# Performance work log

Hardware: AMD Instinct MI355X
Metric: run time of the kernel (lower is better)

Reference implementation:

```python
import jax, jax.numpy as jnp
import numpy as np

B, T, F, H = 2048, 512, 60, 7  # batch, seq_len, input_size, hidden_size


def setup_inputs() -> dict:
    key = jax.random.key(0)
    ks = jax.random.split(key, 9)
    bound = 1.0 / np.sqrt(H)  # PyTorch LSTM init: U(-1/sqrt(H), 1/sqrt(H))
    u = lambda k, s: jax.random.uniform(k, s, jnp.float32, -bound, bound)
    return {
        "x": jax.random.normal(ks[0], (B, T, F), jnp.float32),
        "Wih0": u(ks[1], (4 * H, F)),
        "Whh0": u(ks[2], (4 * H, H)),
        "bih0": u(ks[3], (4 * H,)),
        "bhh0": u(ks[4], (4 * H,)),
        "Wih1": u(ks[5], (4 * H, H)),
        "Whh1": u(ks[6], (4 * H, H)),
        "bih1": u(ks[7], (4 * H,)),
        "bhh1": u(ks[8], (4 * H,)),
    }


def _cell(xt, h, c, Wih, Whh, b):
    # PyTorch gate order: input, forget, cell(g), output
    gates = xt @ Wih.T + h @ Whh.T + b  # [B, 4H]
    i, f, g, o = jnp.split(gates, 4, axis=-1)
    c_new = jax.nn.sigmoid(f) * c + jax.nn.sigmoid(i) * jnp.tanh(g)
    h_new = jax.nn.sigmoid(o) * jnp.tanh(c_new)
    return h_new, c_new


def reference(x, Wih0, Whh0, bih0, bhh0, Wih1, Whh1, bih1, bhh1):
    b0 = bih0 + bhh0
    b1 = bih1 + bhh1
    batch = x.shape[0]
    hid = Whh0.shape[1]
    z = jnp.zeros((batch, hid), x.dtype)

    def step(carry, xt):
        h0, c0, h1, c1 = carry
        h0, c0 = _cell(xt, h0, c0, Wih0, Whh0, b0)
        h1, c1 = _cell(h0, h1, c1, Wih1, Whh1, b1)
        return (h0, c0, h1, c1), None

    xs = jnp.swapaxes(x, 0, 1)  # [T, B, F] for scan over time
    (h0, c0, h1, c1), _ = jax.lax.scan(step, (z, z, z, z), xs)
    # out[:, -1] of batch_first LSTM == final hidden state of top layer
    return h1
```

## Files before the change

kernel.cpp:

```cpp
#include <hip/hip_runtime.h>


#define B_ 2048
#define T_ 512
#define F_ 60
#define H_ 7
#define G4 28
#define CH 16
#define NCH (T_ / CH)
#define F4 15
#define ROW4 (CH * F4)
#define BPB 4
#define TOT4 (BPB * ROW4)
#define L2E 1.4426950408889634f

#if __has_builtin(__builtin_amdgcn_exp2f)
#define EXP2(x) __builtin_amdgcn_exp2f(x)
#else
#define EXP2(x) exp2f(x)
#endif

__device__ __forceinline__ float rcpf_(float v) { return __builtin_amdgcn_rcpf(v); }

__device__ __forceinline__ float bcast(float v, int srclane) {
    return __uint_as_float(__builtin_amdgcn_readlane(__float_as_uint(v), srclane));
}

__device__ __forceinline__ float dot7(const float* w, const float* h, float seed) {
    float m01 = fmaf(w[1], h[1], w[0] * h[0]);
    float m23 = fmaf(w[3], h[3], w[2] * h[2]);
    float m45 = fmaf(w[5], h[5], w[4] * h[4]);
    float m6  = fmaf(w[6], h[6], seed);
    return (m01 + m23) + (m45 + m6);
}

__device__ __forceinline__ float proj32(const float* pw, const float4* rp, float seed) {
    float s0 = seed, s1 = 0.f, s2 = 0.f, s3 = 0.f;
    #pragma unroll
    for (int j = 0; j < 8; ++j) {
        float4 q = rp[j];
        s0 = fmaf(pw[4 * j + 0], q.x, s0);
        s1 = fmaf(pw[4 * j + 1], q.y, s1);
        s2 = fmaf(pw[4 * j + 2], q.z, s2);
        s3 = fmaf(pw[4 * j + 3], q.w, s3);
    }
    return (s0 + s1) + (s2 + s3);
}

__global__ __launch_bounds__(256, 2)
void lstm2_kernel(const float* __restrict__ x,
                  const float* __restrict__ Wih0, const float* __restrict__ Whh0,
                  const float* __restrict__ bih0, const float* __restrict__ bhh0,
                  const float* __restrict__ Wih1, const float* __restrict__ Whh1,
                  const float* __restrict__ bih1, const float* __restrict__ bhh1,
                  float* __restrict__ out)
{
    __shared__ float4 lds4[2][BPB][ROW4];

    const int tid   = threadIdx.x;
    const int lane  = tid & 63;
    const bool isL1 = lane >= 32;
    const int g     = lane & 31;
    const int u     = g;
    const int r     = (g < G4) ? g : (G4 - 1);
    const int grp   = tid >> 6;
    const int b     = blockIdx.x * BPB + grp;

    float pw[32];
    {
        const int offs = isL1 ? 28 : 0;
        #pragma unroll
        for (int k = 0; k < 32; ++k) pw[k] = Wih0[r * F_ + offs + k];
        if (isL1) { pw[0] = pw[1] = pw[2] = pw[3] = 0.f; }
    }
    float wA[H_], wB[H_];
    #pragma unroll
    for (int v = 0; v < H_; ++v) {
        wA[v] = isL1 ? Wih1[r * H_ + v] : Whh0[r * H_ + v];
        wB[v] = isL1 ? Whh1[r * H_ + v] : 0.f;
    }
    const float bias0 = bih0[r] + bhh0[r];
    const float bias1 = bih1[r] + bhh1[r];

    const bool isT = (r >= 2 * H_ && r < 3 * H_);
    const float KK = isT ? (-2.f * L2E) : (-L2E);
    const float Aa = isT ? 2.f : 1.f;
    const float Ca = isT ? -1.f : 0.f;

    float h0v[H_] = {0, 0, 0, 0, 0, 0, 0};
    float h1v[H_] = {0, 0, 0, 0, 0, 0, 0};
    float c = 0.f;
    float hnew = 0.f;

    const float4* __restrict__ xb =
        (const float4*)(x + (size_t)(blockIdx.x * BPB) * T_ * F_);
    const int XB4 = T_ * F4;
    const int lofs = isL1 ? 7 : 0;
    const float pseed = isL1 ? 0.f : bias0;

    #pragma unroll
    for (int i = 0; i < 4; ++i) {
        int idx = tid + 256 * i;
        if (idx < TOT4) {
            int bl = idx / ROW4;
            int j  = idx - bl * ROW4;
            lds4[0][bl][j] = xb[bl * XB4 + j];
        }
    }
    __syncthreads();

    float a_in;
    {
        float ow = proj32(pw, &lds4[0][grp][0] + lofs, pseed);
        a_in = ow + __shfl(ow, lane ^ 32, 64);
    }

    for (int ch = 0; ch < NCH; ++ch) {
        const int cn = (ch < NCH - 1) ? ch + 1 : ch;
        float4 st[4];
        #pragma unroll
        for (int i = 0; i < 4; ++i) {
            int idx = tid + 256 * i;
            if (idx < TOT4) {
                int bl = idx / ROW4;
                int j  = idx - bl * ROW4;
                st[i] = xb[bl * XB4 + cn * ROW4 + j];
            }
        }

        const int buf = ch & 1;
        const float4* __restrict__ rowb = &lds4[buf][grp][0] + lofs;

        #pragma unroll
        for (int s = 0; s < CH; ++s) {
            float seed = isL1 ? bias1 : a_in;
            float a = dot7(wA, h0v, seed);
            a = dot7(wB, h1v, a);
            float act = fmaf(Aa, rcpf_(1.f + EXP2(KK * a)), Ca);

            float fg = __shfl(act, lane + 7, 64);
            float gg = __shfl(act, lane + 14, 64);
            float og = __shfl(act, lane + 21, 64);

            float cnew = fmaf(fg, c, act * gg);
            if (ch == 0 && s == 0) cnew = isL1 ? 0.f : cnew;
            c = cnew;
            float th = fmaf(2.f, rcpf_(1.f + EXP2(-2.f * L2E * c)), -1.f);
            hnew = og * th;

            #pragma unroll
            for (int v = 0; v < H_; ++v) h0v[v] = bcast(hnew, v);
            if (ch > 0 || s > 0) {
                #pragma unroll
                for (int v = 0; v < H_; ++v) h1v[v] = bcast(hnew, 32 + v);
            }

            if (s < CH - 1) {
                float ow = proj32(pw, rowb + (s + 1) * F4, pseed);
                a_in = ow + __shfl(ow, lane ^ 32, 64);
            }
        }

        #pragma unroll
        for (int i = 0; i < 4; ++i) {
            int idx = tid + 256 * i;
            if (idx < TOT4) {
                int bl = idx / ROW4;
                int j  = idx - bl * ROW4;
                lds4[buf ^ 1][bl][j] = st[i];
            }
        }
        __syncthreads();

        if (ch < NCH - 1) {
            float ow = proj32(pw, &lds4[buf ^ 1][grp][0] + lofs, pseed);
            a_in = ow + __shfl(ow, lane ^ 32, 64);
        }
    }

    {
        float seed = isL1 ? bias1 : 0.f;
        float a = dot7(wA, h0v, seed);
        a = dot7(wB, h1v, a);
        float act = fmaf(Aa, rcpf_(1.f + EXP2(KK * a)), Ca);
        float fg = __shfl(act, lane + 7, 64);
        float gg = __shfl(act, lane + 14, 64);
        float og = __shfl(act, lane + 21, 64);
        c = fmaf(fg, c, act * gg);
        float th = fmaf(2.f, rcpf_(1.f + EXP2(-2.f * L2E * c)), -1.f);
        hnew = og * th;
    }

    if (isL1 && u < H_) {
        out[(size_t)b * H_ + u] = hnew;
    }
}

extern "C" void kernel_launch(void* const* d_in, const int* in_sizes, int n_in,
                              void* d_out, int out_size, void* d_ws, size_t ws_size,
                              hipStream_t stream) {
    const float* x    = (const float*)d_in[0];
    const float* Wih0 = (const float*)d_in[1];
    const float* Whh0 = (const float*)d_in[2];
    const float* bih0 = (const float*)d_in[3];
    const float* bhh0 = (const float*)d_in[4];
    const float* Wih1 = (const float*)d_in[5];
    const float* Whh1 = (const float*)d_in[6];
    const float* bih1 = (const float*)d_in[7];
    const float* bhh1 = (const float*)d_in[8];
    float* out = (float*)d_out;

    dim3 grid(B_ / BPB);
    dim3 block(256);
    lstm2_kernel<<<grid, block, 0, stream>>>(x, Wih0, Whh0, bih0, bhh0,
                                             Wih1, Whh1, bih1, bhh1, out);
}
```

Before: 569.8 us.

## Split input projection into a parallel pre-pass kernel before the recurrence

```diff
diff --git a/kernel.cpp b/kernel.cpp
--- a/kernel.cpp
+++ b/kernel.cpp
@@ -6,13 +6,9 @@
 #define F_ 60
 #define H_ 7
 #define G4 28
-#define CH 16
-#define NCH (T_ / CH)
-#define F4 15
-#define ROW4 (CH * F4)
-#define BPB 4
-#define TOT4 (BPB * ROW4)
+#define BT_ (B_ * T_)
 #define L2E 1.4426950408889634f
+#define PD 8
 
 #if __has_builtin(__builtin_amdgcn_exp2f)
 #define EXP2(x) __builtin_amdgcn_exp2f(x)
@@ -34,52 +30,71 @@
     return (m01 + m23) + (m45 + m6);
 }
 
-__device__ __forceinline__ float proj32(const float* pw, const float4* rp, float seed) {
-    float s0 = seed, s1 = 0.f, s2 = 0.f, s3 = 0.f;
-    #pragma unroll
-    for (int j = 0; j < 8; ++j) {
-        float4 q = rp[j];
-        s0 = fmaf(pw[4 * j + 0], q.x, s0);
-        s1 = fmaf(pw[4 * j + 1], q.y, s1);
-        s2 = fmaf(pw[4 * j + 2], q.z, s2);
-        s3 = fmaf(pw[4 * j + 3], q.w, s3);
-    }
-    return (s0 + s1) + (s2 + s3);
-}
-
-__global__ __launch_bounds__(256, 2)
-void lstm2_kernel(const float* __restrict__ x,
-                  const float* __restrict__ Wih0, const float* __restrict__ Whh0,
-                  const float* __restrict__ bih0, const float* __restrict__ bhh0,
-                  const float* __restrict__ Wih1, const float* __restrict__ Whh1,
-                  const float* __restrict__ bih1, const float* __restrict__ bhh1,
-                  float* __restrict__ out)
+__global__ __launch_bounds__(256)
+void proj_kernel(const float* __restrict__ x, const float* __restrict__ Wih0,
+                 const float* __restrict__ bih0, const float* __restrict__ bhh0,
+                 float* __restrict__ A)
 {
-    __shared__ float4 lds4[2][BPB][ROW4];
-
+    __shared__ float wsm[G4 * F_];
+    __shared__ float bsm[G4];
+
+    for (int i = threadIdx.x; i < G4 * F_; i += 256) wsm[i] = Wih0[i];
+    if (threadIdx.x < G4) bsm[threadIdx.x] = bih0[threadIdx.x] + bhh0[threadIdx.x];
+    __syncthreads();
+
+    const int bt = blockIdx.x * 256 + threadIdx.x;
+
+    float xr[F_];
+    const float4* __restrict__ xp = (const float4*)(x + (size_t)bt * F_);
+    #pragma unroll
+    for (int j = 0; j < 15; ++j) {
+        float4 q = xp[j];
+        xr[4 * j + 0] = q.x; xr[4 * j + 1] = q.y;
+        xr[4 * j + 2] = q.z; xr[4 * j + 3] = q.w;
+    }
+
+    float4* __restrict__ Ap = (float4*)(A + (size_t)bt * G4);
+    #pragma unroll
+    for (int rg = 0; rg < 7; ++rg) {
+        float s[4];
+        #pragma unroll
+        for (int q = 0; q < 4; ++q) {
+            const int r = rg * 4 + q;
+            const float* w = &wsm[r * F_];
+            float a0 = bsm[r], a1 = 0.f, a2 = 0.f, a3 = 0.f;
+            #pragma unroll
+            for (int k = 0; k < F_; k += 4) {
+                a0 = fmaf(w[k + 0], xr[k + 0], a0);
+                a1 = fmaf(w[k + 1], xr[k + 1], a1);
+                a2 = fmaf(w[k + 2], xr[k + 2], a2);
+                a3 = fmaf(w[k + 3], xr[k + 3], a3);
+            }
+            s[q] = (a0 + a1) + (a2 + a3);
+        }
+        Ap[rg] = make_float4(s[0], s[1], s[2], s[3]);
+    }
+}
+
+__global__ __launch_bounds__(256)
+void rec_kernel(const float* __restrict__ A,
+                const float* __restrict__ Whh0,
+                const float* __restrict__ Wih1, const float* __restrict__ Whh1,
+                const float* __restrict__ bih1, const float* __restrict__ bhh1,
+                float* __restrict__ out)
+{
     const int tid   = threadIdx.x;
     const int lane  = tid & 63;
     const bool isL1 = lane >= 32;
     const int g     = lane & 31;
-    const int u     = g;
     const int r     = (g < G4) ? g : (G4 - 1);
-    const int grp   = tid >> 6;
-    const int b     = blockIdx.x * BPB + grp;
-
-    float pw[32];
-    {
-        const int offs = isL1 ? 28 : 0;
-        #pragma unroll
-        for (int k = 0; k < 32; ++k) pw[k] = Wih0[r * F_ + offs + k];
-        if (isL1) { pw[0] = pw[1] = pw[2] = pw[3] = 0.f; }
-    }
+    const int b     = blockIdx.x * 4 + (tid >> 6);
+
     float wA[H_], wB[H_];
     #pragma unroll
     for (int v = 0; v < H_; ++v) {
         wA[v] = isL1 ? Wih1[r * H_ + v] : Whh0[r * H_ + v];
         wB[v] = isL1 ? Whh1[r * H_ + v] : 0.f;
     }
-    const float bias0 = bih0[r] + bhh0[r];
     const float bias1 = bih1[r] + bhh1[r];
 
     const bool isT = (r >= 2 * H_ && r < 3 * H_);
@@ -89,51 +104,22 @@
 
     float h0v[H_] = {0, 0, 0, 0, 0, 0, 0};
     float h1v[H_] = {0, 0, 0, 0, 0, 0, 0};
-    float c = 0.f;
-    float hnew = 0.f;
-
-    const float4* __restrict__ xb =
-        (const float4*)(x + (size_t)(blockIdx.x * BPB) * T_ * F_);
-    const int XB4 = T_ * F4;
-    const int lofs = isL1 ? 7 : 0;
-    const float pseed = isL1 ? 0.f : bias0;
-
-    #pragma unroll
-    for (int i = 0; i < 4; ++i) {
-        int idx = tid + 256 * i;
-        if (idx < TOT4) {
-            int bl = idx / ROW4;
-            int j  = idx - bl * ROW4;
-            lds4[0][bl][j] = xb[bl * XB4 + j];
-        }
-    }
-    __syncthreads();
-
-    float a_in;
-    {
-        float ow = proj32(pw, &lds4[0][grp][0] + lofs, pseed);
-        a_in = ow + __shfl(ow, lane ^ 32, 64);
-    }
-
-    for (int ch = 0; ch < NCH; ++ch) {
-        const int cn = (ch < NCH - 1) ? ch + 1 : ch;
-        float4 st[4];
-        #pragma unroll
-        for (int i = 0; i < 4; ++i) {
-            int idx = tid + 256 * i;
-            if (idx < TOT4) {
-                int bl = idx / ROW4;
-                int j  = idx - bl * ROW4;
-                st[i] = xb[bl * XB4 + cn * ROW4 + j];
-            }
-        }
-
-        const int buf = ch & 1;
-        const float4* __restrict__ rowb = &lds4[buf][grp][0] + lofs;
-
-        #pragma unroll
-        for (int s = 0; s < CH; ++s) {
-            float seed = isL1 ? bias1 : a_in;
+    float c = 0.f, hnew = 0.f;
+
+    const float* __restrict__ pa = A + (size_t)b * T_ * G4 + r;
+
+    float buf[PD];
+    #pragma unroll
+    for (int i = 0; i < PD; ++i) buf[i] = pa[i * G4];
+
+    for (int tt = 0; tt < T_; tt += PD) {
+        #pragma unroll
+        for (int s = 0; s < PD; ++s) {
+            const int t = tt + s;
+            const int tn = (t + PD < T_) ? (t + PD) : (T_ - 1);
+            float nb = pa[(size_t)tn * G4];
+
+            float seed = isL1 ? bias1 : buf[s];
             float a = dot7(wA, h0v, seed);
             a = dot7(wB, h1v, a);
             float act = fmaf(Aa, rcpf_(1.f + EXP2(KK * a)), Ca);
@@ -143,44 +129,22 @@
             float og = __shfl(act, lane + 21, 64);
 
             float cnew = fmaf(fg, c, act * gg);
-            if (ch == 0 && s == 0) cnew = isL1 ? 0.f : cnew;
+            if (t == 0) cnew = isL1 ? 0.f : cnew;
             c = cnew;
             float th = fmaf(2.f, rcpf_(1.f + EXP2(-2.f * L2E * c)), -1.f);
             hnew = og * th;
 
             #pragma unroll
             for (int v = 0; v < H_; ++v) h0v[v] = bcast(hnew, v);
-            if (ch > 0 || s > 0) {
-                #pragma unroll
-                for (int v = 0; v < H_; ++v) h1v[v] = bcast(hnew, 32 + v);
-            }
-
-            if (s < CH - 1) {
-                float ow = proj32(pw, rowb + (s + 1) * F4, pseed);
-                a_in = ow + __shfl(ow, lane ^ 32, 64);
-            }
-        }
-
-        #pragma unroll
-        for (int i = 0; i < 4; ++i) {
-            int idx = tid + 256 * i;
-            if (idx < TOT4) {
-                int bl = idx / ROW4;
-                int j  = idx - bl * ROW4;
-                lds4[buf ^ 1][bl][j] = st[i];
-            }
-        }
-        __syncthreads();
-
-        if (ch < NCH - 1) {
-            float ow = proj32(pw, &lds4[buf ^ 1][grp][0] + lofs, pseed);
-            a_in = ow + __shfl(ow, lane ^ 32, 64);
+            #pragma unroll
+            for (int v = 0; v < H_; ++v) h1v[v] = bcast(hnew, 32 + v);
+
+            buf[s] = nb;
         }
     }
 
     {
-        float seed = isL1 ? bias1 : 0.f;
-        float a = dot7(wA, h0v, seed);
+        float a = dot7(wA, h0v, isL1 ? bias1 : 0.f);
         a = dot7(wB, h1v, a);
         float act = fmaf(Aa, rcpf_(1.f + EXP2(KK * a)), Ca);
         float fg = __shfl(act, lane + 7, 64);
@@ -191,9 +155,171 @@
         hnew = og * th;
     }
 
-    if (isL1 && u < H_) {
-        out[(size_t)b * H_ + u] = hnew;
-    }
+    if (isL1 && g < H_) out[(size_t)b * H_ + g] = hnew;
+}
+
+#define CH 16
+#define NCH (T_ / CH)
+#define F4 15
+#define ROW4 (CH * F4)
+#define BPB 4
+#define TOT4 (BPB * ROW4)
+
+__device__ __forceinline__ float proj32(const float* pw, const float4* rp, float seed) {
+    float s0 = seed, s1 = 0.f, s2 = 0.f, s3 = 0.f;
+    #pragma unroll
+    for (int j = 0; j < 8; ++j) {
+        float4 q = rp[j];
+        s0 = fmaf(pw[4 * j + 0], q.x, s0);
+        s1 = fmaf(pw[4 * j + 1], q.y, s1);
+        s2 = fmaf(pw[4 * j + 2], q.z, s2);
+        s3 = fmaf(pw[4 * j + 3], q.w, s3);
+    }
+    return (s0 + s1) + (s2 + s3);
+}
+
+__global__ __launch_bounds__(256, 2)
+void lstm2_fallback(const float* __restrict__ x,
+                    const float* __restrict__ Wih0, const float* __restrict__ Whh0,
+                    const float* __restrict__ bih0, const float* __restrict__ bhh0,
+                    const float* __restrict__ Wih1, const float* __restrict__ Whh1,
+                    const float* __restrict__ bih1, const float* __restrict__ bhh1,
+                    float* __restrict__ out)
+{
+    __shared__ float4 lds4[2][BPB][ROW4];
+
+    const int tid   = threadIdx.x;
+    const int lane  = tid & 63;
+    const bool isL1 = lane >= 32;
+    const int g     = lane & 31;
+    const int r     = (g < G4) ? g : (G4 - 1);
+    const int grp   = tid >> 6;
+    const int b     = blockIdx.x * BPB + grp;
+
+    float pw[32];
+    {
+        const int offs = isL1 ? 28 : 0;
+        #pragma unroll
+        for (int k = 0; k < 32; ++k) pw[k] = Wih0[r * F_ + offs + k];
+        if (isL1) { pw[0] = pw[1] = pw[2] = pw[3] = 0.f; }
+    }
+    float wA[H_], wB[H_];
+    #pragma unroll
+    for (int v = 0; v < H_; ++v) {
+        wA[v] = isL1 ? Wih1[r * H_ + v] : Whh0[r * H_ + v];
+        wB[v] = isL1 ? Whh1[r * H_ + v] : 0.f;
+    }
+    const float bias0 = bih0[r] + bhh0[r];
+    const float bias1 = bih1[r] + bhh1[r];
+
+    const bool isT = (r >= 2 * H_ && r < 3 * H_);
+    const float KK = isT ? (-2.f * L2E) : (-L2E);
+    const float Aa = isT ? 2.f : 1.f;
+    const float Ca = isT ? -1.f : 0.f;
+
+    float h0v[H_] = {0, 0, 0, 0, 0, 0, 0};
+    float h1v[H_] = {0, 0, 0, 0, 0, 0, 0};
+    float c = 0.f, hnew = 0.f;
+
+    const float4* __restrict__ xb =
+        (const float4*)(x + (size_t)(blockIdx.x * BPB) * T_ * F_);
+    const int XB4 = T_ * F4;
+    const int lofs = isL1 ? 7 : 0;
+    const float pseed = isL1 ? 0.f : bias0;
+
+    #pragma unroll
+    for (int i = 0; i < 4; ++i) {
+        int idx = tid + 256 * i;
+        if (idx < TOT4) {
+            int bl = idx / ROW4;
+            int j  = idx - bl * ROW4;
+            lds4[0][bl][j] = xb[bl * XB4 + j];
+        }
+    }
+    __syncthreads();
+
+    float a_in;
+    {
+        float ow = proj32(pw, &lds4[0][grp][0] + lofs, pseed);
+        a_in = ow + __shfl(ow, lane ^ 32, 64);
+    }
+
+    for (int ch = 0; ch < NCH; ++ch) {
+        const int cn = (ch < NCH - 1) ? ch + 1 : ch;
+        float4 st[4];
+        #pragma unroll
+        for (int i = 0; i < 4; ++i) {
+            int idx = tid + 256 * i;
+            if (idx < TOT4) {
+                int bl = idx / ROW4;
+                int j  = idx - bl * ROW4;
+                st[i] = xb[bl * XB4 + cn * ROW4 + j];
+            }
+        }
+
+        const int buf = ch & 1;
+        const float4* __restrict__ rowb = &lds4[buf][grp][0] + lofs;
+
+        #pragma unroll
+        for (int s = 0; s < CH; ++s) {
+            float seed = isL1 ? bias1 : a_in;
+            float a = dot7(wA, h0v, seed);
+            a = dot7(wB, h1v, a);
+            float act = fmaf(Aa, rcpf_(1.f + EXP2(KK * a)), Ca);
+
+            float fg = __shfl(act, lane + 7, 64);
+            float gg = __shfl(act, lane + 14, 64);
+            float og = __shfl(act, lane + 21, 64);
+
+            float cnew = fmaf(fg, c, act * gg);
+            if (ch == 0 && s == 0) cnew = isL1 ? 0.f : cnew;
+            c = cnew;
+            float th = fmaf(2.f, rcpf_(1.f + EXP2(-2.f * L2E * c)), -1.f);
+            hnew = og * th;
+
+            #pragma unroll
+            for (int v = 0; v < H_; ++v) h0v[v] = bcast(hnew, v);
+            if (ch > 0 || s > 0) {
+                #pragma unroll
+                for (int v = 0; v < H_; ++v) h1v[v] = bcast(hnew, 32 + v);
+            }
+
+            if (s < CH - 1) {
+                float ow = proj32(pw, rowb + (s + 1) * F4, pseed);
+                a_in = ow + __shfl(ow, lane ^ 32, 64);
+            }
+        }
+
+        #pragma unroll
+        for (int i = 0; i < 4; ++i) {
+            int idx = tid + 256 * i;
+            if (idx < TOT4) {
+                int bl = idx / ROW4;
+                int j  = idx - bl * ROW4;
+                lds4[buf ^ 1][bl][j] = st[i];
+            }
+        }
+        __syncthreads();
+
+        if (ch < NCH - 1) {
+            float ow = proj32(pw, &lds4[buf ^ 1][grp][0] + lofs, pseed);
+            a_in = ow + __shfl(ow, lane ^ 32, 64);
+        }
+    }
+
+    {
+        float a = dot7(wA, h0v, isL1 ? bias1 : 0.f);
+        a = dot7(wB, h1v, a);
+        float act = fmaf(Aa, rcpf_(1.f + EXP2(KK * a)), Ca);
+        float fg = __shfl(act, lane + 7, 64);
+        float gg = __shfl(act, lane + 14, 64);
+        float og = __shfl(act, lane + 21, 64);
+        c = fmaf(fg, c, act * gg);
+        float th = fmaf(2.f, rcpf_(1.f + EXP2(-2.f * L2E * c)), -1.f);
+        hnew = og * th;
+    }
+
+    if (isL1 && g < H_) out[(size_t)b * H_ + g] = hnew;
 }
 
 extern "C" void kernel_launch(void* const* d_in, const int* in_sizes, int n_in,
@@ -210,8 +336,14 @@
     const float* bhh1 = (const float*)d_in[8];
     float* out = (float*)d_out;
 
-    dim3 grid(B_ / BPB);
-    dim3 block(256);
-    lstm2_kernel<<<grid, block, 0, stream>>>(x, Wih0, Whh0, bih0, bhh0,
-                                             Wih1, Whh1, bih1, bhh1, out);
-}
+    const size_t need = (size_t)BT_ * G4 * sizeof(float);
+    if (ws_size >= need) {
+        float* A = (float*)d_ws;
+        proj_kernel<<<dim3(BT_ / 256), dim3(256), 0, stream>>>(x, Wih0, bih0, bhh0, A);
+        rec_kernel<<<dim3(B_ / 4), dim3(256), 0, stream>>>(A, Whh0, Wih1, Whh1,
+                                                           bih1, bhh1, out);
+    } else {
+        lstm2_fallback<<<dim3(B_ / BPB), dim3(256), 0, stream>>>(
+            x, Wih0, Whh0, bih0, bhh0, Wih1, Whh1, bih1, bhh1, out);
+    }
+}
```

New measurement: 537.5 us. 1.06x faster.
